# Kernel optimization log

Hardware: AMD Instinct MI355X
Metric: run time of the kernel (lower is better)

## Reference

```python
import jax, jax.numpy as jnp
import numpy as np

N_HEADS = 16
ROPE_DIMS = 16
SEQ_LEN = 512


def _rope_cache(T, dtype=jnp.float32):
    rd = ROPE_DIMS
    freqs = 1.0 / (10000.0 ** (jnp.arange(0, rd, 2, dtype=jnp.float32) / rd))  # [rd/2]
    t = jnp.arange(T, dtype=jnp.float32)
    ang = jnp.outer(t, freqs)  # [T, rd/2]
    return jnp.cos(ang).astype(dtype), jnp.sin(ang).astype(dtype)


def _apply_rope(x, cos, sin):
    # x: [B, H, T, hd]; partial RoPE on first ROPE_DIMS dims
    rd = ROPE_DIMS
    x_rope, x_pass = x[..., :rd], x[..., rd:]
    x1, x2 = x_rope[..., : rd // 2], x_rope[..., rd // 2 :]
    # cos/sin: [T, rd/2] -> broadcast over B, H
    out = jnp.concatenate([x1 * cos - x2 * sin, x2 * cos + x1 * sin], axis=-1)
    return jnp.concatenate([out, x_pass], axis=-1)


def setup_inputs() -> dict:
    key = jax.random.key(0)
    k1, k2, k3 = jax.random.split(key, 3)
    B, T, C = 8, SEQ_LEN, 2048
    x = jax.random.normal(k1, (B, T, C), dtype=jnp.float32)
    Wqkv = jax.random.normal(k2, (3 * C, C), dtype=jnp.float32) * (1.0 / np.sqrt(C))
    Wout = jax.random.normal(k3, (C, C), dtype=jnp.float32) * (1.0 / np.sqrt(C))
    return {"x": x, "Wqkv": Wqkv, "Wout": Wout}


def reference(x, Wqkv, Wout):
    B, T, C = x.shape
    H = N_HEADS
    hd = C // H
    # fused QKV projection
    qkv = jnp.einsum("btc,fc->btf", x, Wqkv)  # [B, T, 3C]
    qkv = qkv.reshape(B, T, 3, H, hd)
    q, k, v = qkv[:, :, 0], qkv[:, :, 1], qkv[:, :, 2]  # [B, T, H, hd]
    q = jnp.transpose(q, (0, 2, 1, 3))  # [B, H, T, hd]
    k = jnp.transpose(k, (0, 2, 1, 3))
    v = jnp.transpose(v, (0, 2, 1, 3))
    cos, sin = _rope_cache(T, dtype=x.dtype)
    q = _apply_rope(q, cos, sin)
    k = _apply_rope(k, cos, sin)
    # causal SDPA
    scale = 1.0 / np.sqrt(hd)
    scores = jnp.einsum("bhqd,bhkd->bhqk", q, k) * scale
    causal = jnp.tril(jnp.ones((T, T), dtype=bool))
    scores = jnp.where(causal, scores, jnp.finfo(scores.dtype).min)
    attn = jax.nn.softmax(scores, axis=-1)
    y = jnp.einsum("bhqk,bhkd->bhqd", attn, v)  # [B, H, T, hd]
    y = jnp.transpose(y, (0, 2, 1, 3)).reshape(B, T, C)
    return jnp.einsum("btc,oc->bto", y, Wout)
```

## Files before the change

### kernel.cpp

```cpp
#include <hip/hip_runtime.h>

typedef __bf16 bf16_t;
typedef __bf16 bf16x4 __attribute__((ext_vector_type(4)));
typedef __bf16 bf16x8 __attribute__((ext_vector_type(8)));
typedef float f32x4 __attribute__((ext_vector_type(4)));

#define GLB(p) ((const __attribute__((address_space(1))) void*)(p))
#define LDS(p) ((__attribute__((address_space(3))) void*)(p))

__global__ void f32_to_bf16(const float* __restrict__ src, bf16_t* __restrict__ dst, int n8)
{
    const int i = blockIdx.x * 256 + threadIdx.x;
    if (i >= n8) return;
    const f32x4 a = *(const f32x4*)&src[(size_t)i * 8];
    const f32x4 b = *(const f32x4*)&src[(size_t)i * 8 + 4];
    bf16x8 h = {(bf16_t)a[0], (bf16_t)a[1], (bf16_t)a[2], (bf16_t)a[3],
                (bf16_t)b[0], (bf16_t)b[1], (bf16_t)b[2], (bf16_t)b[3]};
    *(bf16x8*)&dst[(size_t)i * 8] = h;
}

template <int MODE>
__global__ __launch_bounds__(256)
void gemm_bt(const bf16_t* __restrict__ A, const bf16_t* __restrict__ Bm, int K,
             bf16_t* __restrict__ o0, bf16_t* __restrict__ o1, bf16_t* __restrict__ o2,
             float* __restrict__ of)
{
    __shared__ __align__(16) bf16_t As[128 * 32];
    __shared__ __align__(16) bf16_t Bs[128 * 32];
    const int tid  = threadIdx.x;
    const int lane = tid & 63;
    const int w    = tid >> 6;
    const int wm   = (w & 1) * 64;
    const int wn   = (w >> 1) * 64;
    const int m0   = blockIdx.x * 128;
    const int n0   = blockIdx.y * 128;
    const int quad = lane >> 4;
    const int qcol = lane & 15;

    f32x4 acc[4][4];
#pragma unroll
    for (int i = 0; i < 4; ++i)
#pragma unroll
        for (int j = 0; j < 4; ++j)
            acc[i][j] = (f32x4){0.f, 0.f, 0.f, 0.f};

    const int rc = lane >> 2;
    const int cg = (lane & 3) ^ (rc & 3);
    const int c0 = 2 * w, c1 = 2 * w + 1;
    const bf16_t* ag0 = A  + (size_t)(m0 + 16 * c0 + rc) * K + cg * 8;
    const bf16_t* ag1 = A  + (size_t)(m0 + 16 * c1 + rc) * K + cg * 8;
    const bf16_t* bg0 = Bm + (size_t)(n0 + 16 * c0 + rc) * K + cg * 8;
    const bf16_t* bg1 = Bm + (size_t)(n0 + 16 * c1 + rc) * K + cg * 8;
    bf16_t* al0 = &As[c0 * 512];
    bf16_t* al1 = &As[c1 * 512];
    bf16_t* bl0 = &Bs[c0 * 512];
    bf16_t* bl1 = &Bs[c1 * 512];

    const int swz8 = (quad ^ (qcol & 3)) * 8;

    for (int k0 = 0; k0 < K; k0 += 32) {
        __syncthreads();
        __builtin_amdgcn_global_load_lds(GLB(ag0 + k0), LDS(al0), 16, 0, 0);
        __builtin_amdgcn_global_load_lds(GLB(ag1 + k0), LDS(al1), 16, 0, 0);
        __builtin_amdgcn_global_load_lds(GLB(bg0 + k0), LDS(bl0), 16, 0, 0);
        __builtin_amdgcn_global_load_lds(GLB(bg1 + k0), LDS(bl1), 16, 0, 0);
        __syncthreads();

        bf16x8 af[4], bf[4];
#pragma unroll
        for (int mt = 0; mt < 4; ++mt)
            af[mt] = *(const bf16x8*)&As[(wm + mt * 16 + qcol) * 32 + swz8];
#pragma unroll
        for (int nt = 0; nt < 4; ++nt)
            bf[nt] = *(const bf16x8*)&Bs[(wn + nt * 16 + qcol) * 32 + swz8];
#pragma unroll
        for (int mt = 0; mt < 4; ++mt)
#pragma unroll
            for (int nt = 0; nt < 4; ++nt)
                acc[mt][nt] = __builtin_amdgcn_mfma_f32_16x16x32_bf16(af[mt], bf[nt], acc[mt][nt], 0, 0, 0);
    }

#pragma unroll
    for (int mt = 0; mt < 4; ++mt) {
#pragma unroll
        for (int nt = 0; nt < 4; ++nt) {
#pragma unroll
            for (int r = 0; r < 4; ++r) {
                const int m = m0 + wm + mt * 16 + quad * 4 + r;
                const int f = n0 + wn + nt * 16 + qcol;
                const float val = acc[mt][nt][r];
                if (MODE == 0) {
                    const int b     = m >> 9;
                    const int t     = m & 511;
                    const int which = f >> 11;
                    const int h     = (f >> 7) & 15;
                    const int d     = f & 127;
                    if (which == 2) {
                        o2[((size_t)(((b << 4) + h) * 128 + d) << 9) + t] = (bf16_t)val;
                    } else {
                        bf16_t* dst = (which == 0) ? o0 : o1;
                        dst[(size_t)(((b << 4) + h) * 512 + t) * 128 + d] = (bf16_t)val;
                    }
                } else {
                    of[(size_t)m * 2048 + f] = val;
                }
            }
        }
    }
}

__global__ void rope_kernel(bf16_t* __restrict__ q, bf16_t* __restrict__ k)
{
    const int id  = blockIdx.x * 256 + threadIdx.x;
    const int arr = id >> 19;
    const int rem = id & ((1 << 19) - 1);
    const int bh  = rem >> 12;
    const int t   = (rem >> 3) & 511;
    const int d   = rem & 7;

    bf16_t* p = (arr ? k : q) + (size_t)(bh * 512 + t) * 128;
    const float x1 = (float)p[d];
    const float x2 = (float)p[d + 8];
    const float freq = __expf(-(float)d * 1.1512925464970229f);
    const float ang  = (float)t * freq;
    const float c = cosf(ang), s = sinf(ang);
    p[d]     = (bf16_t)(x1 * c - x2 * s);
    p[d + 8] = (bf16_t)(x2 * c + x1 * s);
}

#define KLD 136
#define VLD 72
#define PLD 72

__global__ __launch_bounds__(256)
void flash_attn(const bf16_t* __restrict__ q, const bf16_t* __restrict__ k,
                const bf16_t* __restrict__ vT, bf16_t* __restrict__ y)
{
    const int qt = blockIdx.x;
    const int h  = blockIdx.y;
    const int b  = blockIdx.z;
    const int tid  = threadIdx.x;
    const int lane = tid & 63;
    const int w    = tid >> 6;
    const int quad = lane >> 4;
    const int qcol = lane & 15;

    __shared__ __align__(16) bf16_t Ks[64 * KLD];
    __shared__ __align__(16) bf16_t VTs[128 * VLD];
    __shared__ __align__(16) bf16_t Ps[64 * PLD];
    __shared__ __align__(16) float aS[4][16];
    __shared__ __align__(16) float lS[4][16];

    const bf16_t* qb  = q  + (size_t)((b * 16 + h) * 512) * 128;
    const bf16_t* kb  = k  + (size_t)((b * 16 + h) * 512) * 128;
    const bf16_t* vtb = vT + (size_t)((b * 16 + h) * 128) * 512;

    bf16x8 qfrag[4];
    const int qrow = qt * 64 + w * 16 + qcol;
#pragma unroll
    for (int kc = 0; kc < 4; ++kc)
        qfrag[kc] = *(const bf16x8*)&qb[(size_t)qrow * 128 + kc * 32 + quad * 8];

    f32x4 acc_o[8];
#pragma unroll
    for (int nt = 0; nt < 8; ++nt) acc_o[nt] = (f32x4){0.f, 0.f, 0.f, 0.f};
    float m_run = -INFINITY, l_run = 0.f;
    const float scale = 0.08838834764831845f;

    for (int kt = 0; kt <= qt; ++kt) {
        __syncthreads();
#pragma unroll
        for (int p = 0; p < 4; ++p) {
            const int r = p * 16 + (tid >> 4), c = (tid & 15) * 8;
            *(uint4*)&Ks[r * KLD + c] = *(const uint4*)&kb[(size_t)(kt * 64 + r) * 128 + c];
        }
#pragma unroll
        for (int p = 0; p < 4; ++p) {
            const int r = p * 32 + (tid >> 3), c = (tid & 7) * 8;
            *(uint4*)&VTs[r * VLD + c] = *(const uint4*)&vtb[(size_t)r * 512 + kt * 64 + c];
        }
        __syncthreads();

        f32x4 sacc[4];
#pragma unroll
        for (int mt = 0; mt < 4; ++mt) sacc[mt] = (f32x4){0.f, 0.f, 0.f, 0.f};
#pragma unroll
        for (int mt = 0; mt < 4; ++mt)
#pragma unroll
            for (int kc = 0; kc < 4; ++kc) {
                bf16x8 af = *(const bf16x8*)&Ks[(mt * 16 + qcol) * KLD + kc * 32 + quad * 8];
                sacc[mt] = __builtin_amdgcn_mfma_f32_16x16x32_bf16(af, qfrag[kc], sacc[mt], 0, 0, 0);
            }

        float s[16];
#pragma unroll
        for (int mt = 0; mt < 4; ++mt)
#pragma unroll
            for (int r = 0; r < 4; ++r)
                s[mt * 4 + r] = sacc[mt][r] * scale;
        if (kt == qt) {
#pragma unroll
            for (int mt = 0; mt < 4; ++mt)
#pragma unroll
                for (int r = 0; r < 4; ++r)
                    if (mt * 16 + quad * 4 + r > w * 16 + qcol)
                        s[mt * 4 + r] = -1e30f;
        }

        float mx = s[0];
#pragma unroll
        for (int i = 1; i < 16; ++i) mx = fmaxf(mx, s[i]);
        mx = fmaxf(mx, __shfl_xor(mx, 16));
        mx = fmaxf(mx, __shfl_xor(mx, 32));
        const float m_new = fmaxf(m_run, mx);
        const float alpha = __expf(m_run - m_new);
        float p16[16];
        float sum = 0.f;
#pragma unroll
        for (int i = 0; i < 16; ++i) { p16[i] = __expf(s[i] - m_new); sum += p16[i]; }
        sum += __shfl_xor(sum, 16);
        sum += __shfl_xor(sum, 32);
        l_run = l_run * alpha + sum;
        m_run = m_new;
        if (quad == 0) aS[w][qcol] = alpha;

#pragma unroll
        for (int mt = 0; mt < 4; ++mt) {
            bf16x4 pb = {(bf16_t)p16[mt * 4 + 0], (bf16_t)p16[mt * 4 + 1],
                         (bf16_t)p16[mt * 4 + 2], (bf16_t)p16[mt * 4 + 3]};
            *(bf16x4*)&Ps[(w * 16 + qcol) * PLD + mt * 16 + quad * 4] = pb;
        }

        f32x4 alpha4 = *(const f32x4*)&aS[w][quad * 4];
#pragma unroll
        for (int nt = 0; nt < 8; ++nt)
#pragma unroll
            for (int r = 0; r < 4; ++r)
                acc_o[nt][r] *= alpha4[r];

#pragma unroll
        for (int kc2 = 0; kc2 < 2; ++kc2) {
            bf16x8 pf = *(const bf16x8*)&Ps[(w * 16 + qcol) * PLD + kc2 * 32 + quad * 8];
#pragma unroll
            for (int nt = 0; nt < 8; ++nt) {
                bf16x8 vf = *(const bf16x8*)&VTs[(nt * 16 + qcol) * VLD + kc2 * 32 + quad * 8];
                acc_o[nt] = __builtin_amdgcn_mfma_f32_16x16x32_bf16(pf, vf, acc_o[nt], 0, 0, 0);
            }
        }
    }

    if (quad == 0) lS[w][qcol] = l_run;
    f32x4 l4 = *(const f32x4*)&lS[w][quad * 4];
#pragma unroll
    for (int nt = 0; nt < 8; ++nt)
#pragma unroll
        for (int r = 0; r < 4; ++r) {
            const int t  = qt * 64 + w * 16 + quad * 4 + r;
            const int cc = h * 128 + nt * 16 + qcol;
            y[(size_t)(b * 512 + t) * 2048 + cc] = (bf16_t)(acc_o[nt][r] / l4[r]);
        }
}

extern "C" void kernel_launch(void* const* d_in, const int* in_sizes, int n_in,
                              void* d_out, int out_size, void* d_ws, size_t ws_size,
                              hipStream_t stream)
{
    (void)in_sizes; (void)n_in; (void)out_size; (void)ws_size;

    const float* x    = (const float*)d_in[0];
    const float* Wqkv = (const float*)d_in[1];
    const float* Wout = (const float*)d_in[2];
    float* out = (float*)d_out;

    const size_t SEG = (size_t)8 * 16 * 512 * 128;
    bf16_t* q      = (bf16_t*)d_ws;
    bf16_t* k      = q + SEG;
    bf16_t* vT     = k + SEG;
    bf16_t* xb     = vT + SEG;
    bf16_t* y      = xb;
    bf16_t* Wqkvb  = xb + SEG;
    bf16_t* Woutb  = Wqkvb + (size_t)6144 * 2048;

    f32_to_bf16<<<(8388608 / 8) / 256, 256, 0, stream>>>(x, xb, 8388608 / 8);
    f32_to_bf16<<<(12582912 / 8) / 256, 256, 0, stream>>>(Wqkv, Wqkvb, 12582912 / 8);
    f32_to_bf16<<<(4194304 / 8) / 256, 256, 0, stream>>>(Wout, Woutb, 4194304 / 8);
    gemm_bt<0><<<dim3(4096 / 128, 6144 / 128), 256, 0, stream>>>(xb, Wqkvb, 2048, q, k, vT, nullptr);
    rope_kernel<<<(2 * 128 * 512 * 8) / 256, 256, 0, stream>>>(q, k);
    flash_attn<<<dim3(8, 16, 8), 256, 0, stream>>>(q, k, vT, y);
    gemm_bt<1><<<dim3(4096 / 128, 2048 / 128), 256, 0, stream>>>(y, Woutb, 2048, nullptr, nullptr, nullptr, out);
}
```

Measured before the change: 391.3 us.

## Process 128 query rows per flash-attention block to reuse K/V tiles

Each flash-attention block now handles 128 query rows instead of 64, with each wave owning two 16-row query groups that share every K/V tile loaded into LDS. This halves the grid and the global-to-LDS K/V traffic per query row. In exchange it raises register pressure with doubled accumulators and query fragments, and it does more wasted masked work on diagonal tiles. The coarser grid also gives worse causal load balance and fewer blocks to hide latency.

```diff
diff --git a/kernel.cpp b/kernel.cpp
--- a/kernel.cpp
+++ b/kernel.cpp
@@ -136,9 +136,9 @@
 void flash_attn(const bf16_t* __restrict__ q, const bf16_t* __restrict__ k,
                 const bf16_t* __restrict__ vT, bf16_t* __restrict__ y)
 {
-    const int qt = blockIdx.x;
-    const int h  = blockIdx.y;
-    const int b  = blockIdx.z;
+    const int qtb = blockIdx.x;
+    const int h   = blockIdx.y;
+    const int b   = blockIdx.z;
     const int tid  = threadIdx.x;
     const int lane = tid & 63;
     const int w    = tid >> 6;
@@ -147,27 +147,34 @@
 
     __shared__ __align__(16) bf16_t Ks[64 * KLD];
     __shared__ __align__(16) bf16_t VTs[128 * VLD];
-    __shared__ __align__(16) bf16_t Ps[64 * PLD];
-    __shared__ __align__(16) float aS[4][16];
-    __shared__ __align__(16) float lS[4][16];
+    __shared__ __align__(16) bf16_t Ps[128 * PLD];
+    __shared__ __align__(16) float aS[4][2][16];
+    __shared__ __align__(16) float lS[4][2][16];
 
     const bf16_t* qb  = q  + (size_t)((b * 16 + h) * 512) * 128;
     const bf16_t* kb  = k  + (size_t)((b * 16 + h) * 512) * 128;
     const bf16_t* vtb = vT + (size_t)((b * 16 + h) * 128) * 512;
 
-    bf16x8 qfrag[4];
-    const int qrow = qt * 64 + w * 16 + qcol;
-#pragma unroll
-    for (int kc = 0; kc < 4; ++kc)
-        qfrag[kc] = *(const bf16x8*)&qb[(size_t)qrow * 128 + kc * 32 + quad * 8];
-
-    f32x4 acc_o[8];
-#pragma unroll
-    for (int nt = 0; nt < 8; ++nt) acc_o[nt] = (f32x4){0.f, 0.f, 0.f, 0.f};
-    float m_run = -INFINITY, l_run = 0.f;
+    bf16x8 qfrag[2][4];
+#pragma unroll
+    for (int qg = 0; qg < 2; ++qg) {
+        const int qrow = qtb * 128 + w * 32 + qg * 16 + qcol;
+#pragma unroll
+        for (int kc = 0; kc < 4; ++kc)
+            qfrag[qg][kc] = *(const bf16x8*)&qb[(size_t)qrow * 128 + kc * 32 + quad * 8];
+    }
+
+    f32x4 acc_o[2][8];
+#pragma unroll
+    for (int qg = 0; qg < 2; ++qg)
+#pragma unroll
+        for (int nt = 0; nt < 8; ++nt) acc_o[qg][nt] = (f32x4){0.f, 0.f, 0.f, 0.f};
+    float m_run[2] = {-INFINITY, -INFINITY};
+    float l_run[2] = {0.f, 0.f};
     const float scale = 0.08838834764831845f;
 
-    for (int kt = 0; kt <= qt; ++kt) {
+    const int kt_last = 2 * qtb + 1;
+    for (int kt = 0; kt <= kt_last; ++kt) {
         __syncthreads();
 #pragma unroll
         for (int p = 0; p < 4; ++p) {
@@ -181,84 +188,93 @@
         }
         __syncthreads();
 
-        f32x4 sacc[4];
-#pragma unroll
-        for (int mt = 0; mt < 4; ++mt) sacc[mt] = (f32x4){0.f, 0.f, 0.f, 0.f};
-#pragma unroll
-        for (int mt = 0; mt < 4; ++mt)
-#pragma unroll
-            for (int kc = 0; kc < 4; ++kc) {
-                bf16x8 af = *(const bf16x8*)&Ks[(mt * 16 + qcol) * KLD + kc * 32 + quad * 8];
-                sacc[mt] = __builtin_amdgcn_mfma_f32_16x16x32_bf16(af, qfrag[kc], sacc[mt], 0, 0, 0);
-            }
-
-        float s[16];
-#pragma unroll
-        for (int mt = 0; mt < 4; ++mt)
-#pragma unroll
-            for (int r = 0; r < 4; ++r)
-                s[mt * 4 + r] = sacc[mt][r] * scale;
-        if (kt == qt) {
+        const bool need_mask = (kt >= 2 * qtb);
+
+#pragma unroll
+        for (int qg = 0; qg < 2; ++qg) {
+            f32x4 sacc[4];
+#pragma unroll
+            for (int mt = 0; mt < 4; ++mt) sacc[mt] = (f32x4){0.f, 0.f, 0.f, 0.f};
 #pragma unroll
             for (int mt = 0; mt < 4; ++mt)
 #pragma unroll
+                for (int kc = 0; kc < 4; ++kc) {
+                    bf16x8 af = *(const bf16x8*)&Ks[(mt * 16 + qcol) * KLD + kc * 32 + quad * 8];
+                    sacc[mt] = __builtin_amdgcn_mfma_f32_16x16x32_bf16(af, qfrag[qg][kc], sacc[mt], 0, 0, 0);
+                }
+
+            float s[16];
+#pragma unroll
+            for (int mt = 0; mt < 4; ++mt)
+#pragma unroll
                 for (int r = 0; r < 4; ++r)
-                    if (mt * 16 + quad * 4 + r > w * 16 + qcol)
-                        s[mt * 4 + r] = -1e30f;
+                    s[mt * 4 + r] = sacc[mt][r] * scale;
+            if (need_mask) {
+                const int qglob = qtb * 128 + w * 32 + qg * 16 + qcol;
+#pragma unroll
+                for (int mt = 0; mt < 4; ++mt)
+#pragma unroll
+                    for (int r = 0; r < 4; ++r)
+                        if (kt * 64 + mt * 16 + quad * 4 + r > qglob)
+                            s[mt * 4 + r] = -1e30f;
+            }
+
+            float mx = s[0];
+#pragma unroll
+            for (int i = 1; i < 16; ++i) mx = fmaxf(mx, s[i]);
+            mx = fmaxf(mx, __shfl_xor(mx, 16));
+            mx = fmaxf(mx, __shfl_xor(mx, 32));
+            const float m_new = fmaxf(m_run[qg], mx);
+            const float alpha = __expf(m_run[qg] - m_new);
+            float p16[16];
+            float sum = 0.f;
+#pragma unroll
+            for (int i = 0; i < 16; ++i) { p16[i] = __expf(s[i] - m_new); sum += p16[i]; }
+            sum += __shfl_xor(sum, 16);
+            sum += __shfl_xor(sum, 32);
+            l_run[qg] = l_run[qg] * alpha + sum;
+            m_run[qg] = m_new;
+            if (quad == 0) aS[w][qg][qcol] = alpha;
+
+#pragma unroll
+            for (int mt = 0; mt < 4; ++mt) {
+                bf16x4 pb = {(bf16_t)p16[mt * 4 + 0], (bf16_t)p16[mt * 4 + 1],
+                             (bf16_t)p16[mt * 4 + 2], (bf16_t)p16[mt * 4 + 3]};
+                *(bf16x4*)&Ps[(w * 32 + qg * 16 + qcol) * PLD + mt * 16 + quad * 4] = pb;
+            }
+
+            f32x4 alpha4 = *(const f32x4*)&aS[w][qg][quad * 4];
+#pragma unroll
+            for (int nt = 0; nt < 8; ++nt)
+#pragma unroll
+                for (int r = 0; r < 4; ++r)
+                    acc_o[qg][nt][r] *= alpha4[r];
+
+#pragma unroll
+            for (int kc2 = 0; kc2 < 2; ++kc2) {
+                bf16x8 pf = *(const bf16x8*)&Ps[(w * 32 + qg * 16 + qcol) * PLD + kc2 * 32 + quad * 8];
+#pragma unroll
+                for (int nt = 0; nt < 8; ++nt) {
+                    bf16x8 vf = *(const bf16x8*)&VTs[(nt * 16 + qcol) * VLD + kc2 * 32 + quad * 8];
+                    acc_o[qg][nt] = __builtin_amdgcn_mfma_f32_16x16x32_bf16(pf, vf, acc_o[qg][nt], 0, 0, 0);
+                }
+            }
         }
-
-        float mx = s[0];
-#pragma unroll
-        for (int i = 1; i < 16; ++i) mx = fmaxf(mx, s[i]);
-        mx = fmaxf(mx, __shfl_xor(mx, 16));
-        mx = fmaxf(mx, __shfl_xor(mx, 32));
-        const float m_new = fmaxf(m_run, mx);
-        const float alpha = __expf(m_run - m_new);
-        float p16[16];
-        float sum = 0.f;
-#pragma unroll
-        for (int i = 0; i < 16; ++i) { p16[i] = __expf(s[i] - m_new); sum += p16[i]; }
-        sum += __shfl_xor(sum, 16);
-        sum += __shfl_xor(sum, 32);
-        l_run = l_run * alpha + sum;
-        m_run = m_new;
-        if (quad == 0) aS[w][qcol] = alpha;
-
-#pragma unroll
-        for (int mt = 0; mt < 4; ++mt) {
-            bf16x4 pb = {(bf16_t)p16[mt * 4 + 0], (bf16_t)p16[mt * 4 + 1],
-                         (bf16_t)p16[mt * 4 + 2], (bf16_t)p16[mt * 4 + 3]};
-            *(bf16x4*)&Ps[(w * 16 + qcol) * PLD + mt * 16 + quad * 4] = pb;
-        }
-
-        f32x4 alpha4 = *(const f32x4*)&aS[w][quad * 4];
+    }
+
+    if (quad == 0) { lS[w][0][qcol] = l_run[0]; lS[w][1][qcol] = l_run[1]; }
+#pragma unroll
+    for (int qg = 0; qg < 2; ++qg) {
+        f32x4 l4 = *(const f32x4*)&lS[w][qg][quad * 4];
 #pragma unroll
         for (int nt = 0; nt < 8; ++nt)
 #pragma unroll
-            for (int r = 0; r < 4; ++r)
-                acc_o[nt][r] *= alpha4[r];
-
-#pragma unroll
-        for (int kc2 = 0; kc2 < 2; ++kc2) {
-            bf16x8 pf = *(const bf16x8*)&Ps[(w * 16 + qcol) * PLD + kc2 * 32 + quad * 8];
-#pragma unroll
-            for (int nt = 0; nt < 8; ++nt) {
-                bf16x8 vf = *(const bf16x8*)&VTs[(nt * 16 + qcol) * VLD + kc2 * 32 + quad * 8];
-                acc_o[nt] = __builtin_amdgcn_mfma_f32_16x16x32_bf16(pf, vf, acc_o[nt], 0, 0, 0);
-            }
-        }
-    }
-
-    if (quad == 0) lS[w][qcol] = l_run;
-    f32x4 l4 = *(const f32x4*)&lS[w][quad * 4];
-#pragma unroll
-    for (int nt = 0; nt < 8; ++nt)
-#pragma unroll
-        for (int r = 0; r < 4; ++r) {
-            const int t  = qt * 64 + w * 16 + quad * 4 + r;
-            const int cc = h * 128 + nt * 16 + qcol;
-            y[(size_t)(b * 512 + t) * 2048 + cc] = (bf16_t)(acc_o[nt][r] / l4[r]);
-        }
+            for (int r = 0; r < 4; ++r) {
+                const int t  = qtb * 128 + w * 32 + qg * 16 + quad * 4 + r;
+                const int cc = h * 128 + nt * 16 + qcol;
+                y[(size_t)(b * 512 + t) * 2048 + cc] = (bf16_t)(acc_o[qg][nt][r] / l4[r]);
+            }
+    }
 }
 
 extern "C" void kernel_launch(void* const* d_in, const int* in_sizes, int n_in,
@@ -286,6 +302,6 @@
     f32_to_bf16<<<(4194304 / 8) / 256, 256, 0, stream>>>(Wout, Woutb, 4194304 / 8);
     gemm_bt<0><<<dim3(4096 / 128, 6144 / 128), 256, 0, stream>>>(xb, Wqkvb, 2048, q, k, vT, nullptr);
     rope_kernel<<<(2 * 128 * 512 * 8) / 256, 256, 0, stream>>>(q, k);
-    flash_attn<<<dim3(8, 16, 8), 256, 0, stream>>>(q, k, vT, y);
+    flash_attn<<<dim3(4, 16, 8), 256, 0, stream>>>(q, k, vT, y);
     gemm_bt<1><<<dim3(4096 / 128, 2048 / 128), 256, 0, stream>>>(y, Woutb, 2048, nullptr, nullptr, nullptr, out);
 }
```

After: 375.6 us. 4.0% less time.
